# Optimization experiments

Hardware: AMD Instinct MI355X
Metric: run time of the kernel (lower is better)

## Reference

```python
import jax, jax.numpy as jnp
import numpy as np

E = 8          # num_experts
K = 2          # top_k
CAPF = 1.25    # capacity_factor
DIM = 512
HID = 2048     # int(dim * mlp_ratio)


def setup_inputs() -> dict:
    key = jax.random.key(0)
    ks = jax.random.split(key, 5)
    s = 0.02
    x = jax.random.normal(ks[0], (8, 2048, DIM), jnp.float32)
    Wr = jax.random.normal(ks[1], (E, DIM), jnp.float32) * s          # router weight (no bias)
    W1 = jax.random.normal(ks[2], (E, HID, DIM), jnp.float32) * s     # fc1 weights per expert
    b1 = jnp.zeros((E, HID), jnp.float32)
    W2 = jax.random.normal(ks[3], (E, DIM, HID), jnp.float32) * s     # fc2 weights per expert
    b2 = jnp.zeros((E, DIM), jnp.float32)
    return {"x": x, "Wr": Wr, "W1": W1, "b1": b1, "W2": W2, "b2": b2}


def _capacity_keep(top_w, top_idx, cap):
    """For each (slot, expert), keep only the `cap` highest-weight tokens.
    top_w, top_idx: [T, K]. Returns bool keep mask [T, K]."""
    def per_slot(w, idx):
        order = jnp.argsort(-w)                       # tokens sorted by weight desc
        idx_sorted = idx[order]                       # [T] expert id in sorted order
        oh = jax.nn.one_hot(idx_sorted, E, dtype=jnp.int32)
        rank = jnp.cumsum(oh, axis=0) - 1             # rank within each expert
        r = jnp.take_along_axis(rank, idx_sorted[:, None], axis=1)[:, 0]
        keep_sorted = r < cap
        return jnp.zeros(w.shape[0], bool).at[order].set(keep_sorted)
    return jax.vmap(per_slot, in_axes=(1, 1), out_axes=1)(top_w, top_idx)


def reference(x, Wr, W1, b1, W2, b2):
    b, n, d = x.shape
    T = b * n
    flat = x.reshape(T, d)

    # Router: softmax in fp32 then cast back
    logits = flat @ Wr.T                                            # [T, E]
    probs = jax.nn.softmax(logits.astype(jnp.float32), axis=-1).astype(flat.dtype)
    top_w, top_idx = jax.lax.top_k(probs, K)                        # [T, K]
    top_w = top_w / (jnp.sum(top_w, axis=-1, keepdims=True) + 1e-8)

    # Capacity-limited drop, then renormalize
    cap = max(1, int(CAPF * T * K / E))
    keep = _capacity_keep(top_w, top_idx, cap)
    top_w = jnp.where(keep, top_w, 0.0)
    top_w = top_w / jnp.clip(jnp.sum(top_w, axis=-1, keepdims=True), 1e-8, None)

    # Combine weight per (token, expert): scatter-add top_w into dense [T, E]
    rows = jnp.arange(T)[:, None]
    w_te = jnp.zeros((T, E), flat.dtype).at[rows, top_idx].add(top_w)

    # Per-expert MLP, weighted combine (w_te is 0 for unassigned/dropped pairs)
    out = jnp.zeros_like(flat)
    for e in range(E):
        h = jax.nn.gelu(flat @ W1[e].T + b1[e], approximate=False)  # [T, HID]
        y = h @ W2[e].T + b2[e]                                     # [T, D]
        out = out + w_te[:, e:e + 1] * y

    # Load-balancing aux loss
    load = jnp.sum(w_te, axis=0) / T
    importance = probs.mean(0)
    aux = jnp.sum(importance * load * float(E))
    return out.reshape(b, n, d), aux
```

## Files before the change

### kernel.cpp

```cpp
#include <hip/hip_runtime.h>
#include <hip/hip_bf16.h>
#include <math.h>

#define DIM 512
#define HID 2048
#define NE  8
#define CSTRIDE 32

typedef __attribute__((ext_vector_type(8))) short short8;
typedef __attribute__((ext_vector_type(4))) float f32x4;
typedef unsigned short ushort_t;

static __device__ __forceinline__ ushort_t f2bf(float f) {
    unsigned int x = __builtin_bit_cast(unsigned int, f);
    unsigned int lsb = (x >> 16) & 1u;
    x += 0x7fffu + lsb;
    return (ushort_t)(x >> 16);
}
static __device__ __forceinline__ float bf2f(ushort_t u) {
    unsigned int x = ((unsigned int)u) << 16;
    return __builtin_bit_cast(float, x);
}

static __device__ __forceinline__ float fast_gelu(float v) {
    float u = v * 0.70710678118654752f;
    float s = fabsf(u);
    float t = __builtin_amdgcn_rcpf(1.f + 0.3275911f * s);
    float poly = ((((1.061405429f * t - 1.453152027f) * t + 1.421413741f) * t
                   - 0.284496736f) * t + 0.254829592f) * t;
    float e = __expf(-s * s);
    float erfv = copysignf(1.f - poly * e, u);
    return 0.5f * v * (1.f + erfv);
}

static __device__ __forceinline__ void gld16(const void* g, void* l) {
    __builtin_amdgcn_global_load_lds(
        (const __attribute__((address_space(1))) void*)g,
        (__attribute__((address_space(3))) void*)l,
        16, 0, 0);
}

__global__ void k_cvt2(const float* __restrict__ s1, ushort_t* __restrict__ d1, int n1,
                       const float* __restrict__ s2, ushort_t* __restrict__ d2, int n2) {
    int i = blockIdx.x * blockDim.x + threadIdx.x;
    int stride = gridDim.x * blockDim.x;
    int n4a = n1 >> 2, n4b = n2 >> 2;
    for (int j = i; j < n4a; j += stride) {
        float4 v = ((const float4*)s1)[j];
        ushort4 o;
        o.x = f2bf(v.x); o.y = f2bf(v.y); o.z = f2bf(v.z); o.w = f2bf(v.w);
        ((ushort4*)d1)[j] = o;
    }
    for (int j = i; j < n4b; j += stride) {
        float4 v = ((const float4*)s2)[j];
        ushort4 o;
        o.x = f2bf(v.x); o.y = f2bf(v.y); o.z = f2bf(v.z); o.w = f2bf(v.w);
        ((ushort4*)d2)[j] = o;
    }
}

__global__ __launch_bounds__(256) void k_router(const float* __restrict__ x,
    const float* __restrict__ Wr, ushort_t* __restrict__ xb,
    float* __restrict__ probs, int* __restrict__ tidx, float* __restrict__ tw, int T)
{
    int lane = threadIdx.x & 63;
    int t = blockIdx.x * 4 + (threadIdx.x >> 6);
    if (t >= T) return;
    const float* xr = x + (size_t)t * DIM;
    double acc[NE];
#pragma unroll
    for (int e = 0; e < NE; e++) acc[e] = 0.0;
    for (int i = lane; i < DIM; i += 64) {
        float xv = xr[i];
        xb[(size_t)t * DIM + i] = f2bf(xv);
        double xd = (double)xv;
#pragma unroll
        for (int e = 0; e < NE; e++) acc[e] += xd * (double)Wr[e * DIM + i];
    }
#pragma unroll
    for (int e = 0; e < NE; e++) {
#pragma unroll
        for (int off = 32; off > 0; off >>= 1) acc[e] += __shfl_xor(acc[e], off);
    }
    double mx = acc[0];
#pragma unroll
    for (int e = 1; e < NE; e++) mx = fmax(mx, acc[e]);
    double p[NE], sum = 0.0;
#pragma unroll
    for (int e = 0; e < NE; e++) { p[e] = exp(acc[e] - mx); sum += p[e]; }
    float pr[NE];
#pragma unroll
    for (int e = 0; e < NE; e++) pr[e] = (float)(p[e] / sum);
    if (lane < NE) probs[(size_t)t * NE + lane] = pr[lane];
    if (lane == 0) {
        int i1 = 0; float b1v = pr[0];
#pragma unroll
        for (int e = 1; e < NE; e++) if (pr[e] > b1v) { b1v = pr[e]; i1 = e; }
        int i2 = -1; float b2v = -1.f;
#pragma unroll
        for (int e = 0; e < NE; e++) if (e != i1 && pr[e] > b2v) { b2v = pr[e]; i2 = e; }
        float s2 = b1v + b2v + 1e-8f;
        tidx[t * 2] = i1; tidx[t * 2 + 1] = i2;
        tw[t * 2] = b1v / s2; tw[t * 2 + 1] = b2v / s2;
    }
}

__global__ __launch_bounds__(256) void k_hist(const int* __restrict__ tidx,
                                              int* __restrict__ cnt, int T) {
    __shared__ int h[16];
    if (threadIdx.x < 16) h[threadIdx.x] = 0;
    __syncthreads();
    int stride = gridDim.x * blockDim.x;
    for (int t = blockIdx.x * blockDim.x + threadIdx.x; t < T; t += stride) {
        atomicAdd(&h[tidx[t * 2]], 1);
        atomicAdd(&h[8 + tidx[t * 2 + 1]], 1);
    }
    __syncthreads();
    if (threadIdx.x < 16 && h[threadIdx.x] != 0)
        atomicAdd(&cnt[threadIdx.x * CSTRIDE], h[threadIdx.x]);
}

__global__ __launch_bounds__(256) void k_post(const int* __restrict__ tidx,
        const float* __restrict__ tw, const int* __restrict__ cnt,
        const float* __restrict__ probs, int* __restrict__ lcnt,
        int* __restrict__ ltok, int* __restrict__ pos, float* __restrict__ tw2,
        float* __restrict__ partial, int T, int cap, int capM)
{
    __shared__ int h[NE];
    __shared__ int base[NE];
    __shared__ float red[256 * 16];
    if (threadIdx.x < NE) h[threadIdx.x] = 0;
    __syncthreads();
    int t = blockIdx.x * blockDim.x + threadIdx.x;
    float wkn[2] = {0.f, 0.f};
    int myE[2] = {-1, -1};
    int myp[2] = {0, 0};
    if (t < T) {
        float wk[2]; int es[2];
#pragma unroll
        for (int s = 0; s < 2; s++) {
            int e = tidx[t * 2 + s];
            float w = tw[t * 2 + s];
            es[s] = e; wk[s] = w;
            if (cnt[(s * NE + e) * CSTRIDE] > cap) {
                int rank = 0;
                for (int t2 = 0; t2 < T; t2++) {
                    if (tidx[t2 * 2 + s] == e) {
                        float w2 = tw[t2 * 2 + s];
                        if (w2 > w || (w2 == w && t2 < t)) rank++;
                    }
                }
                if (rank >= cap) wk[s] = 0.f;
            }
        }
        float denom = fmaxf(wk[0] + wk[1], 1e-8f);
#pragma unroll
        for (int s = 0; s < 2; s++) {
            wkn[s] = wk[s] / denom;
            tw2[t * 2 + s] = wkn[s];
            if (wkn[s] != 0.f) {
                myE[s] = es[s];
                myp[s] = atomicAdd(&h[es[s]], 1);
            }
        }
    }
    __syncthreads();
    if (threadIdx.x < NE)
        base[threadIdx.x] = (h[threadIdx.x] != 0)
            ? atomicAdd(&lcnt[threadIdx.x * CSTRIDE], h[threadIdx.x]) : 0;
    __syncthreads();
    float imp[NE], ld[NE];
#pragma unroll
    for (int e = 0; e < NE; e++) { imp[e] = 0.f; ld[e] = 0.f; }
    if (t < T) {
#pragma unroll
        for (int s = 0; s < 2; s++) {
            if (myE[s] >= 0) {
                int p = base[myE[s]] + myp[s];
                ltok[myE[s] * capM + p] = t;
                pos[t * 2 + s] = (myE[s] << 20) | p;
                ld[myE[s]] += wkn[s];
            } else {
                pos[t * 2 + s] = -1;
            }
        }
#pragma unroll
        for (int e = 0; e < NE; e++) imp[e] = probs[(size_t)t * NE + e];
    }
#pragma unroll
    for (int e = 0; e < NE; e++) {
        red[threadIdx.x * 16 + e] = imp[e];
        red[threadIdx.x * 16 + 8 + e] = ld[e];
    }
    __syncthreads();
    for (int off = 128; off > 0; off >>= 1) {
        if (threadIdx.x < off) {
#pragma unroll
            for (int j = 0; j < 16; j++)
                red[threadIdx.x * 16 + j] += red[(threadIdx.x + off) * 16 + j];
        }
        __syncthreads();
    }
    if (threadIdx.x < 16) partial[blockIdx.x * 16 + threadIdx.x] = red[threadIdx.x];
}

__global__ void k_tail(const int* __restrict__ lcnt, int* __restrict__ loff,
                       const float* __restrict__ partial, float* __restrict__ outaux,
                       int nb, int T)
{
    __shared__ float s[16];
    if (threadIdx.x == 0) {
        int o = 0;
        for (int e = 0; e < NE; e++) {
            loff[e] = o;
            o += ((lcnt[e * CSTRIDE] + 127) >> 7) << 7;
        }
        loff[NE] = o;
    }
    if (threadIdx.x < 16) {
        float a = 0.f;
        for (int b = 0; b < nb; b++) a += partial[b * 16 + threadIdx.x];
        s[threadIdx.x] = a;
    }
    __syncthreads();
    if (threadIdx.x == 0) {
        float invT = 1.f / (float)T;
        float aux = 0.f;
        for (int e = 0; e < NE; e++)
            aux += (s[e] * invT) * (s[8 + e] * invT) * (float)NE;
        outaux[0] = aux;
    }
}

__global__ __launch_bounds__(256, 2) void k_fc1(
    const ushort_t* __restrict__ xb, const ushort_t* __restrict__ W1b,
    const float* __restrict__ b1, const int* __restrict__ lcnt,
    const int* __restrict__ loff, const int* __restrict__ ltok,
    ushort_t* __restrict__ hbuf, int capM)
{
    int bx = blockIdx.x;
    int e  = bx & 7;
    int r  = bx >> 3;
    int mt = r >> 4;
    int nt = r & 15;
    int cnt = lcnt[e * CSTRIDE];
    if (cnt > capM) cnt = capM;
    int m0 = mt * 128;
    if (m0 >= cnt) return;
    int n0 = nt * 128;
    const int* toks = ltok + e * capM;
    int hrow0 = loff[e] + m0;
    const ushort_t* Bsrc = W1b + (size_t)e * HID * DIM;

    __shared__ char smem[65536];
    char* As0 = smem;          char* Bs0 = smem + 16384;
    char* As1 = smem + 32768;  char* Bs1 = smem + 49152;

    int tid = threadIdx.x;
    int wave = tid >> 6, lane = tid & 63;
    int wm = wave >> 1, wn = wave & 1;

    const char* aSrc[4]; const char* bSrc[4]; int ldst[4];
#pragma unroll
    for (int i = 0; i < 4; i++) {
        int c = tid + 256 * i;
        int row = c >> 3, cc = c & 7;
        int scc = cc ^ (row & 7);
        int gr = m0 + row;
        int tok = toks[gr < cnt ? gr : (cnt - 1)];
        aSrc[i] = (const char*)(xb + (size_t)tok * DIM + scc * 8);
        bSrc[i] = (const char*)(Bsrc + (size_t)(n0 + row) * DIM + scc * 8);
        ldst[i] = (i * 256 + wave * 64) * 16;
    }

    f32x4 acc[4][4];
#pragma unroll
    for (int a = 0; a < 4; a++)
#pragma unroll
        for (int b = 0; b < 4; b++) acc[a][b] = (f32x4){0.f, 0.f, 0.f, 0.f};

    int aRow = wm * 64 + (lane & 15);
    int bRow = wn * 64 + (lane & 15);
    int kq = lane >> 4;
    int swz0 = (kq ^ (lane & 7)) << 4;
    int swz1 = ((4 + kq) ^ (lane & 7)) << 4;
    int aoff[2] = { aRow * 128 + swz0, aRow * 128 + swz1 };
    int boff[2] = { bRow * 128 + swz0, bRow * 128 + swz1 };

    auto STAGE = [&](int kofs, char* A, char* B) {
#pragma unroll
        for (int i = 0; i < 4; i++) {
            gld16(aSrc[i] + kofs, A + ldst[i]);
            gld16(bSrc[i] + kofs, B + ldst[i]);
        }
    };
    auto COMPUTE = [&](const char* A, const char* B) {
#pragma unroll
        for (int kk = 0; kk < 2; kk++) {
            short8 af[4], bfr[4];
#pragma unroll
            for (int mf = 0; mf < 4; mf++)
                af[mf] = *(const short8*)(A + aoff[kk] + mf * 2048);
#pragma unroll
            for (int nf = 0; nf < 4; nf++)
                bfr[nf] = *(const short8*)(B + boff[kk] + nf * 2048);
#pragma unroll
            for (int mf = 0; mf < 4; mf++)
#pragma unroll
                for (int nf = 0; nf < 4; nf++)
                    acc[mf][nf] = __builtin_amdgcn_mfma_f32_16x16x32_bf16(bfr[nf], af[mf], acc[mf][nf], 0, 0, 0);
        }
    };

    const int NT = DIM / 64;
    STAGE(0, As0, Bs0);
#pragma unroll
    for (int t = 0; t < NT; t++) {
        char* Ac = (t & 1) ? As1 : As0;
        char* Bc = (t & 1) ? Bs1 : Bs0;
        if (t + 1 < NT) {
            STAGE((t + 1) * 128, (t & 1) ? As0 : As1, (t & 1) ? Bs0 : Bs1);
            asm volatile("s_waitcnt vmcnt(8)" ::: "memory");
        } else {
            asm volatile("s_waitcnt vmcnt(0)" ::: "memory");
        }
        __builtin_amdgcn_s_barrier();
        __builtin_amdgcn_sched_barrier(0);
        COMPUTE(Ac, Bc);
        __builtin_amdgcn_sched_barrier(0);
        __builtin_amdgcn_s_barrier();
    }

    const float* b1e = b1 + e * HID;
    int mlocal = wm * 64 + (lane & 15);
    int nbase0 = n0 + wn * 64 + (lane >> 4) * 4;
#pragma unroll
    for (int mf = 0; mf < 4; mf++) {
        int mrow = mlocal + mf * 16;
        bool valid = (m0 + mrow) < cnt;
        ushort_t* dst = hbuf + (size_t)(hrow0 + mrow) * HID;
#pragma unroll
        for (int nf = 0; nf < 4; nf++) {
            int nc = nbase0 + nf * 16;
            float4 bias4 = *(const float4*)(b1e + nc);
            ushort4 o;
            o.x = f2bf(fast_gelu(acc[mf][nf][0] + bias4.x));
            o.y = f2bf(fast_gelu(acc[mf][nf][1] + bias4.y));
            o.z = f2bf(fast_gelu(acc[mf][nf][2] + bias4.z));
            o.w = f2bf(fast_gelu(acc[mf][nf][3] + bias4.w));
            if (valid) *(ushort4*)(dst + nc) = o;
        }
    }
}

__global__ __launch_bounds__(256, 2) void k_fc2(
    const ushort_t* __restrict__ hbuf, const ushort_t* __restrict__ W2b,
    const float* __restrict__ b2, const int* __restrict__ lcnt,
    const int* __restrict__ loff, ushort_t* __restrict__ ybuf, int capM)
{
    int bx = blockIdx.x;
    int e  = bx & 7;
    int r  = bx >> 3;
    int mt = r >> 2;
    int nt = r & 3;
    int cnt = lcnt[e * CSTRIDE];
    if (cnt > capM) cnt = capM;
    int m0 = mt * 128;
    if (m0 >= cnt) return;
    int n0 = nt * 128;
    int hrow0 = loff[e] + m0;
    const ushort_t* Bsrc = W2b + (size_t)e * DIM * HID;

    __shared__ char smem[65536];
    char* As0 = smem;          char* Bs0 = smem + 16384;
    char* As1 = smem + 32768;  char* Bs1 = smem + 49152;

    int tid = threadIdx.x;
    int wave = tid >> 6, lane = tid & 63;
    int wm = wave >> 1, wn = wave & 1;

    const char* aSrc[4]; const char* bSrc[4]; int ldst[4];
#pragma unroll
    for (int i = 0; i < 4; i++) {
        int c = tid + 256 * i;
        int row = c >> 3, cc = c & 7;
        int scc = cc ^ (row & 7);
        aSrc[i] = (const char*)(hbuf + (size_t)(hrow0 + row) * HID + scc * 8);
        bSrc[i] = (const char*)(Bsrc + (size_t)(n0 + row) * HID + scc * 8);
        ldst[i] = (i * 256 + wave * 64) * 16;
    }

    f32x4 acc[4][4];
#pragma unroll
    for (int a = 0; a < 4; a++)
#pragma unroll
        for (int b = 0; b < 4; b++) acc[a][b] = (f32x4){0.f, 0.f, 0.f, 0.f};

    int aRow = wm * 64 + (lane & 15);
    int bRow = wn * 64 + (lane & 15);
    int kq = lane >> 4;
    int swz0 = (kq ^ (lane & 7)) << 4;
    int swz1 = ((4 + kq) ^ (lane & 7)) << 4;
    int aoff[2] = { aRow * 128 + swz0, aRow * 128 + swz1 };
    int boff[2] = { bRow * 128 + swz0, bRow * 128 + swz1 };

    auto STAGE = [&](int kofs, char* A, char* B) {
#pragma unroll
        for (int i = 0; i < 4; i++) {
            gld16(aSrc[i] + kofs, A + ldst[i]);
            gld16(bSrc[i] + kofs, B + ldst[i]);
        }
    };
    auto COMPUTE = [&](const char* A, const char* B) {
#pragma unroll
        for (int kk = 0; kk < 2; kk++) {
            short8 af[4], bfr[4];
#pragma unroll
            for (int mf = 0; mf < 4; mf++)
                af[mf] = *(const short8*)(A + aoff[kk] + mf * 2048);
#pragma unroll
            for (int nf = 0; nf < 4; nf++)
                bfr[nf] = *(const short8*)(B + boff[kk] + nf * 2048);
#pragma unroll
            for (int mf = 0; mf < 4; mf++)
#pragma unroll
                for (int nf = 0; nf < 4; nf++)
                    acc[mf][nf] = __builtin_amdgcn_mfma_f32_16x16x32_bf16(bfr[nf], af[mf], acc[mf][nf], 0, 0, 0);
        }
    };

    const int NT = HID / 64;
    STAGE(0, As0, Bs0);
#pragma unroll
    for (int t = 0; t < NT; t++) {
        char* Ac = (t & 1) ? As1 : As0;
        char* Bc = (t & 1) ? Bs1 : Bs0;
        if (t + 1 < NT) {
            STAGE((t + 1) * 128, (t & 1) ? As0 : As1, (t & 1) ? Bs0 : Bs1);
            asm volatile("s_waitcnt vmcnt(8)" ::: "memory");
        } else {
            asm volatile("s_waitcnt vmcnt(0)" ::: "memory");
        }
        __builtin_amdgcn_s_barrier();
        __builtin_amdgcn_sched_barrier(0);
        COMPUTE(Ac, Bc);
        __builtin_amdgcn_sched_barrier(0);
        __builtin_amdgcn_s_barrier();
    }

    const float* b2e = b2 + e * DIM;
    int mlocal = wm * 64 + (lane & 15);
    int nbase0 = n0 + wn * 64 + (lane >> 4) * 4;
#pragma unroll
    for (int mf = 0; mf < 4; mf++) {
        int mrow = mlocal + mf * 16;
        bool valid = (m0 + mrow) < cnt;
        ushort_t* dst = ybuf + (size_t)(hrow0 + mrow) * DIM;
#pragma unroll
        for (int nf = 0; nf < 4; nf++) {
            int nc = nbase0 + nf * 16;
            float4 bias4 = *(const float4*)(b2e + nc);
            ushort4 o;
            o.x = f2bf(acc[mf][nf][0] + bias4.x);
            o.y = f2bf(acc[mf][nf][1] + bias4.y);
            o.z = f2bf(acc[mf][nf][2] + bias4.z);
            o.w = f2bf(acc[mf][nf][3] + bias4.w);
            if (valid) *(ushort4*)(dst + nc) = o;
        }
    }
}

__global__ __launch_bounds__(256) void k_comb(const ushort_t* __restrict__ ybuf,
    const float* __restrict__ tw2, const int* __restrict__ pos,
    const int* __restrict__ loff, float* __restrict__ out, int T, int capM)
{
    int wv = threadIdx.x >> 6, lane = threadIdx.x & 63;
    int t = blockIdx.x * 4 + wv;
    if (t >= T) return;
    float o[8];
#pragma unroll
    for (int j = 0; j < 8; j++) o[j] = 0.f;
#pragma unroll
    for (int s = 0; s < 2; s++) {
        int pk = pos[t * 2 + s];
        if (pk >= 0) {
            float w = tw2[t * 2 + s];
            int e = pk >> 20, p = pk & 0xFFFFF;
            int row = loff[e] + p;
            short8 y = *(const short8*)(ybuf + (size_t)row * DIM + lane * 8);
#pragma unroll
            for (int j = 0; j < 8; j++) o[j] += w * bf2f((ushort_t)y[j]);
        }
    }
    float4* dst = (float4*)(out + (size_t)t * DIM + lane * 8);
    dst[0] = (float4){o[0], o[1], o[2], o[3]};
    dst[1] = (float4){o[4], o[5], o[6], o[7]};
}

extern "C" void kernel_launch(void* const* d_in, const int* in_sizes, int n_in,
                              void* d_out, int out_size, void* d_ws, size_t ws_size,
                              hipStream_t stream)
{
    const float* x  = (const float*)d_in[0];
    const float* Wr = (const float*)d_in[1];
    const float* W1 = (const float*)d_in[2];
    const float* b1 = (const float*)d_in[3];
    const float* W2 = (const float*)d_in[4];
    const float* b2 = (const float*)d_in[5];
    float* out = (float*)d_out;

    int T = in_sizes[0] / DIM;
    int cap = (int)(1.25 * (double)T * 2.0 / 8.0);
    if (cap < 1) cap = 1;
    int capM = 2 * cap; if (capM > T) capM = T;
    int mtmax = (capM + 127) / 128;
    int nposts = (T + 255) / 256;

    char* w = (char*)d_ws;
    size_t off = 0;
    auto alloc = [&](size_t bytes) {
        char* p = w + off;
        off = (off + bytes + 255) & ~(size_t)255;
        return p;
    };
    size_t ybrows = (size_t)T * 2 + NE * 128;
    size_t ybbytes = ybrows * DIM * 2;
    ushort_t* ybuf = (ushort_t*)w;
    ushort_t* xb   = (ushort_t*)alloc((size_t)T * DIM * 2);
    ushort_t* W1b  = (ushort_t*)alloc((size_t)NE * HID * DIM * 2);
    if (off < ybbytes) off = (ybbytes + 255) & ~(size_t)255;
    ushort_t* W2b  = (ushort_t*)alloc((size_t)NE * DIM * HID * 2);
    ushort_t* hbuf = (ushort_t*)alloc(ybrows * HID * 2);
    float* probs   = (float*)alloc((size_t)T * NE * 4);
    int*   tidx    = (int*)alloc((size_t)T * 2 * 4);
    float* tw      = (float*)alloc((size_t)T * 2 * 4);
    float* tw2     = (float*)alloc((size_t)T * 2 * 4);
    int*   pos     = (int*)alloc((size_t)T * 2 * 4);
    int*   cnt     = (int*)alloc(16 * CSTRIDE * 4);
    int*   lcnt    = (int*)alloc(NE * CSTRIDE * 4);
    int*   loff    = (int*)alloc((NE + 1) * 4);
    int*   ltok    = (int*)alloc((size_t)NE * capM * 4);
    float* partial = (float*)alloc((size_t)nposts * 16 * 4);

    (void)hipMemsetAsync(cnt, 0, 16 * CSTRIDE * 4, stream);
    (void)hipMemsetAsync(lcnt, 0, NE * CSTRIDE * 4, stream);

    k_cvt2<<<2048, 256, 0, stream>>>(W1, W1b, NE * HID * DIM, W2, W2b, NE * DIM * HID);
    k_router<<<(T + 3) / 4, 256, 0, stream>>>(x, Wr, xb, probs, tidx, tw, T);
    k_hist<<<64, 256, 0, stream>>>(tidx, cnt, T);
    k_post<<<nposts, 256, 0, stream>>>(tidx, tw, cnt, probs, lcnt, ltok, pos, tw2,
                                       partial, T, cap, capM);
    k_tail<<<1, 64, 0, stream>>>(lcnt, loff, partial, out + (size_t)T * DIM, nposts, T);

    k_fc1<<<NE * mtmax * (HID / 128), 256, 0, stream>>>(
        xb, W1b, b1, lcnt, loff, ltok, hbuf, capM);
    k_fc2<<<NE * mtmax * (DIM / 128), 256, 0, stream>>>(
        hbuf, W2b, b2, lcnt, loff, ybuf, capM);
    k_comb<<<(T + 3) / 4, 256, 0, stream>>>(ybuf, tw2, pos, loff, out, T, capM);
}
```

Baseline: 275.9 us.

## Merge weight conversion with router kernel and use LUT-interpolated GELU in fc1

```diff
diff --git a/kernel.cpp b/kernel.cpp
--- a/kernel.cpp
+++ b/kernel.cpp
@@ -6,6 +6,7 @@
 #define HID 2048
 #define NE  8
 #define CSTRIDE 32
+#define CVTB 1024
 
 typedef __attribute__((ext_vector_type(8))) short short8;
 typedef __attribute__((ext_vector_type(4))) float f32x4;
@@ -22,7 +23,7 @@
     return __builtin_bit_cast(float, x);
 }
 
-static __device__ __forceinline__ float fast_gelu(float v) {
+static __device__ __forceinline__ float phi_as(float v) {
     float u = v * 0.70710678118654752f;
     float s = fabsf(u);
     float t = __builtin_amdgcn_rcpf(1.f + 0.3275911f * s);
@@ -30,7 +31,7 @@
                    - 0.284496736f) * t + 0.254829592f) * t;
     float e = __expf(-s * s);
     float erfv = copysignf(1.f - poly * e, u);
-    return 0.5f * v * (1.f + erfv);
+    return 0.5f * (1.f + erfv);
 }
 
 static __device__ __forceinline__ void gld16(const void* g, void* l) {
@@ -40,31 +41,33 @@
         16, 0, 0);
 }
 
-__global__ void k_cvt2(const float* __restrict__ s1, ushort_t* __restrict__ d1, int n1,
-                       const float* __restrict__ s2, ushort_t* __restrict__ d2, int n2) {
-    int i = blockIdx.x * blockDim.x + threadIdx.x;
-    int stride = gridDim.x * blockDim.x;
-    int n4a = n1 >> 2, n4b = n2 >> 2;
-    for (int j = i; j < n4a; j += stride) {
-        float4 v = ((const float4*)s1)[j];
-        ushort4 o;
-        o.x = f2bf(v.x); o.y = f2bf(v.y); o.z = f2bf(v.z); o.w = f2bf(v.w);
-        ((ushort4*)d1)[j] = o;
-    }
-    for (int j = i; j < n4b; j += stride) {
-        float4 v = ((const float4*)s2)[j];
-        ushort4 o;
-        o.x = f2bf(v.x); o.y = f2bf(v.y); o.z = f2bf(v.z); o.w = f2bf(v.w);
-        ((ushort4*)d2)[j] = o;
-    }
-}
-
-__global__ __launch_bounds__(256) void k_router(const float* __restrict__ x,
-    const float* __restrict__ Wr, ushort_t* __restrict__ xb,
-    float* __restrict__ probs, int* __restrict__ tidx, float* __restrict__ tw, int T)
-{
+__global__ __launch_bounds__(256) void k_init(
+    const float* __restrict__ W1, ushort_t* __restrict__ W1b, int n1,
+    const float* __restrict__ W2, ushort_t* __restrict__ W2b, int n2,
+    const float* __restrict__ x, const float* __restrict__ Wr,
+    ushort_t* __restrict__ xb, float* __restrict__ probs,
+    int* __restrict__ tidx, float* __restrict__ tw, int T)
+{
+    if (blockIdx.x < CVTB) {
+        int i = blockIdx.x * 256 + threadIdx.x;
+        int stride = CVTB * 256;
+        int n4a = n1 >> 2, n4b = n2 >> 2;
+        for (int j = i; j < n4a; j += stride) {
+            float4 v = ((const float4*)W1)[j];
+            ushort4 o;
+            o.x = f2bf(v.x); o.y = f2bf(v.y); o.z = f2bf(v.z); o.w = f2bf(v.w);
+            ((ushort4*)W1b)[j] = o;
+        }
+        for (int j = i; j < n4b; j += stride) {
+            float4 v = ((const float4*)W2)[j];
+            ushort4 o;
+            o.x = f2bf(v.x); o.y = f2bf(v.y); o.z = f2bf(v.z); o.w = f2bf(v.w);
+            ((ushort4*)W2b)[j] = o;
+        }
+        return;
+    }
     int lane = threadIdx.x & 63;
-    int t = blockIdx.x * 4 + (threadIdx.x >> 6);
+    int t = (blockIdx.x - CVTB) * 4 + (threadIdx.x >> 6);
     if (t >= T) return;
     const float* xr = x + (size_t)t * DIM;
     double acc[NE];
@@ -253,12 +256,20 @@
     const ushort_t* Bsrc = W1b + (size_t)e * HID * DIM;
 
     __shared__ char smem[65536];
+    __shared__ float lut[1024];
     char* As0 = smem;          char* Bs0 = smem + 16384;
     char* As1 = smem + 32768;  char* Bs1 = smem + 49152;
 
     int tid = threadIdx.x;
     int wave = tid >> 6, lane = tid & 63;
     int wm = wave >> 1, wn = wave & 1;
+
+#pragma unroll
+    for (int i = 0; i < 4; i++) {
+        int idx = tid + 256 * i;
+        lut[idx] = phi_as(-6.f + (float)idx * 0.01171875f);
+    }
+    __syncthreads();
 
     const char* aSrc[4]; const char* bSrc[4]; int ldst[4];
 #pragma unroll
@@ -344,10 +355,17 @@
             int nc = nbase0 + nf * 16;
             float4 bias4 = *(const float4*)(b1e + nc);
             ushort4 o;
-            o.x = f2bf(fast_gelu(acc[mf][nf][0] + bias4.x));
-            o.y = f2bf(fast_gelu(acc[mf][nf][1] + bias4.y));
-            o.z = f2bf(fast_gelu(acc[mf][nf][2] + bias4.z));
-            o.w = f2bf(fast_gelu(acc[mf][nf][3] + bias4.w));
+#pragma unroll
+            for (int rr = 0; rr < 4; rr++) {
+                float v = acc[mf][nf][rr] + ((const float*)&bias4)[rr];
+                float xf = fmaf(v, 85.333336f, 512.0f);
+                xf = fminf(fmaxf(xf, 0.f), 1022.99f);
+                int ii = (int)xf;
+                float ffr = xf - (float)ii;
+                float y0 = lut[ii], y1 = lut[ii + 1];
+                float g = v * fmaf(ffr, y1 - y0, y0);
+                ((ushort_t*)&o)[rr] = f2bf(g);
+            }
             if (valid) *(ushort4*)(dst + nc) = o;
         }
     }
@@ -545,8 +563,10 @@
     (void)hipMemsetAsync(cnt, 0, 16 * CSTRIDE * 4, stream);
     (void)hipMemsetAsync(lcnt, 0, NE * CSTRIDE * 4, stream);
 
-    k_cvt2<<<2048, 256, 0, stream>>>(W1, W1b, NE * HID * DIM, W2, W2b, NE * DIM * HID);
-    k_router<<<(T + 3) / 4, 256, 0, stream>>>(x, Wr, xb, probs, tidx, tw, T);
+    int nrb = (T + 3) / 4;
+    k_init<<<CVTB + nrb, 256, 0, stream>>>(W1, W1b, NE * HID * DIM,
+                                           W2, W2b, NE * DIM * HID,
+                                           x, Wr, xb, probs, tidx, tw, T);
     k_hist<<<64, 256, 0, stream>>>(tidx, cnt, T);
     k_post<<<nposts, 256, 0, stream>>>(tidx, tw, cnt, probs, lcnt, ltok, pos, tw2,
                                        partial, T, cap, capM);
```

Result: no change. 279.6 us (+1.3%).
